# Kernel tuning notes

Measured on AMD Instinct MI355X. Metric: run time of the kernel, lower is better.

The kernel has to match this reference:

```python
import jax, jax.numpy as jnp
import numpy as np

EMBED_DIM = 1024


def setup_inputs() -> dict:
    key = jax.random.key(0)
    ks = jax.random.split(key, 8)
    B, S, D = 4, 2048, EMBED_DIM
    scale = 1.0 / np.sqrt(D)
    x = jax.random.normal(ks[0], (B, S, D), dtype=jnp.float32)
    mask = jnp.zeros((S, S), dtype=jnp.float32)
    # nn.Linear default init ~ U(-1/sqrt(fan_in), 1/sqrt(fan_in)); exact dist irrelevant for correctness
    w_q = jax.random.uniform(ks[1], (D, D), jnp.float32, -scale, scale)
    b_q = jax.random.uniform(ks[2], (D,), jnp.float32, -scale, scale)
    w_k = jax.random.uniform(ks[3], (D, D), jnp.float32, -scale, scale)
    b_k = jax.random.uniform(ks[4], (D,), jnp.float32, -scale, scale)
    w_v = jax.random.uniform(ks[5], (D, D), jnp.float32, -scale, scale)
    b_v = jax.random.uniform(ks[6], (D,), jnp.float32, -scale, scale)
    return {"x": x, "mask": mask, "w_q": w_q, "b_q": b_q,
            "w_k": w_k, "b_k": b_k, "w_v": w_v, "b_v": b_v}


def reference(x, mask, w_q, b_q, w_k, b_k, w_v, b_v):
    D = x.shape[-1]
    # nn.Linear computes x @ W^T + b
    Q = jnp.einsum('bsd,ed->bse', x, w_q) + b_q
    K = jnp.einsum('bsd,ed->bse', x, w_k) + b_k
    V = jnp.einsum('bsd,ed->bse', x, w_v) + b_v
    scores = jnp.einsum('bqd,bkd->bqk', Q, K) / jnp.sqrt(jnp.asarray(D, x.dtype))
    scores = scores + mask  # additive mask, broadcast over batch
    attn = jax.nn.softmax(scores, axis=-1)
    return jnp.einsum('bqk,bkd->bqd', attn, V)
```

## Files before the change

kernel.cpp:

```cpp
#include <hip/hip_runtime.h>


typedef __attribute__((ext_vector_type(8))) short short8;
typedef __attribute__((ext_vector_type(4))) short short4v;
typedef __attribute__((ext_vector_type(4))) float float4v;

__device__ __forceinline__ short f2bf(float f) {
  unsigned u = __builtin_bit_cast(unsigned, f);
  u += 0x7fffu + ((u >> 16) & 1u);
  return (short)(u >> 16);
}
__device__ __forceinline__ float bf2f(short s) {
  unsigned u = ((unsigned)(unsigned short)s) << 16;
  return __builtin_bit_cast(float, u);
}

__device__ __forceinline__ void gl2lds16(const void* g, void* l) {
  __builtin_amdgcn_global_load_lds((const __attribute__((address_space(1))) void*)g,
                                   (__attribute__((address_space(3))) void*)l, 16, 0, 0);
}

__global__ __launch_bounds__(256) void prep_kernel(const float* __restrict__ x,
                                                   const float* __restrict__ wq,
                                                   const float* __restrict__ wk,
                                                   const float* __restrict__ wv,
                                                   const float* __restrict__ bq,
                                                   const float* __restrict__ bk,
                                                   short* __restrict__ x_bf,
                                                   short* __restrict__ w_bf,
                                                   float* __restrict__ bcat) {
  int b = blockIdx.x;
  if (b < 3072) {
    int seg = b >> 10;
    const float* w = seg == 0 ? wq : (seg == 1 ? wk : wv);
    int i = (b - (seg << 10)) * 256 + threadIdx.x;
    float4v v = ((const float4v*)w)[i];
    short4v o;
    o.x = f2bf(v.x); o.y = f2bf(v.y); o.z = f2bf(v.z); o.w = f2bf(v.w);
    ((short4v*)(w_bf + (long)seg * 1048576))[i] = o;
  } else if (b < 11264) {
    int i = (b - 3072) * 256 + threadIdx.x;
    float4v v = ((const float4v*)x)[i];
    short4v o;
    o.x = f2bf(v.x); o.y = f2bf(v.y); o.z = f2bf(v.z); o.w = f2bf(v.w);
    ((short4v*)x_bf)[i] = o;
  } else {
    int i = (b - 11264) * 256 + threadIdx.x;
    if (i < 2048) bcat[i] = i < 1024 ? bq[i] : bk[i - 1024];
  }
}

__device__ __forceinline__ void stage_half(const short* __restrict__ g, int ld,
                                           int grow0, int kt, short* lds, int t) {
  const int r = t >> 3;
  const int cch = (t & 7) ^ (r & 7);
  const long co = (long)kt + cch * 8;
  gl2lds16(g + (long)(grow0 + r) * ld + co, lds + t * 8);
  gl2lds16(g + (long)(grow0 + 64 + r) * ld + co, lds + 4096 + t * 8);
}

template <int EPI>
__device__ __forceinline__ void gemm_body(const short* __restrict__ A,
                                          const short* __restrict__ Bm,
                                          void* __restrict__ C,
                                          const float* __restrict__ aux,
                                          float* __restrict__ rsum, float scale,
                                          int N, int Kd, int Bld, int m0, int n0,
                                          short (*As)[64], short (*Bs)[64]) {
  const int t = threadIdx.x;
  const int lane = t & 63;
  const int wave = t >> 6;
  const int wm = (wave >> 2) * 128;
  const int wn = (wave & 3) * 64;
  const int col = lane & 15, quad = lane >> 4;
  const int sw = col & 7;
  const int NT = Kd >> 6;

  float4v acc[8][4] = {};

  stage_half(A, Kd, m0, 0, &As[0][0], t);
  stage_half(A, Kd, m0 + 128, 0, &As[128][0], t);
  stage_half(Bm, Bld, n0, 0, &Bs[0][0], t);
  stage_half(Bm, Bld, n0 + 128, 0, &Bs[128][0], t);
  if (NT > 1) {
    stage_half(Bm, Bld, n0, 64, &Bs[256][0], t);
    stage_half(Bm, Bld, n0 + 128, 64, &Bs[384][0], t);
    asm volatile("s_waitcnt vmcnt(4)" ::: "memory");
  } else {
    asm volatile("s_waitcnt vmcnt(0)" ::: "memory");
  }
  __builtin_amdgcn_s_barrier();

#pragma unroll 2
  for (int k = 0; k < NT; ++k) {
    const int buf = (k & 1) << 8;
    const int nbf = 256 - buf;
    short8 a[4][2], b0[2][2], b1[2][2];

#pragma unroll
    for (int i = 0; i < 4; ++i)
#pragma unroll
      for (int s = 0; s < 2; ++s)
        a[i][s] = *(const short8*)&As[buf + wm + i * 16 + col][(((s * 4 + quad) ^ sw)) * 8];
#pragma unroll
    for (int j = 0; j < 2; ++j)
#pragma unroll
      for (int s = 0; s < 2; ++s)
        b0[j][s] = *(const short8*)&Bs[buf + wn + j * 16 + col][(((s * 4 + quad) ^ sw)) * 8];
    if (k + 1 < NT) stage_half(A, Kd, m0, (k + 1) * 64, &As[nbf][0], t);
    __builtin_amdgcn_s_barrier();
    __builtin_amdgcn_s_setprio(1);
#pragma unroll
    for (int i = 0; i < 4; ++i)
#pragma unroll
      for (int j = 0; j < 2; ++j)
#pragma unroll
        for (int s = 0; s < 2; ++s)
          acc[i][j] = __builtin_amdgcn_mfma_f32_16x16x32_bf16(a[i][s], b0[j][s], acc[i][j], 0, 0, 0);
    __builtin_amdgcn_s_setprio(0);
    __builtin_amdgcn_s_barrier();

#pragma unroll
    for (int j = 0; j < 2; ++j)
#pragma unroll
      for (int s = 0; s < 2; ++s)
        b1[j][s] = *(const short8*)&Bs[buf + wn + (j + 2) * 16 + col][(((s * 4 + quad) ^ sw)) * 8];
    if (k + 1 < NT) stage_half(A, Kd, m0 + 128, (k + 1) * 64, &As[nbf + 128][0], t);
    __builtin_amdgcn_s_barrier();
    __builtin_amdgcn_s_setprio(1);
#pragma unroll
    for (int i = 0; i < 4; ++i)
#pragma unroll
      for (int j = 0; j < 2; ++j)
#pragma unroll
        for (int s = 0; s < 2; ++s)
          acc[i][j + 2] = __builtin_amdgcn_mfma_f32_16x16x32_bf16(a[i][s], b1[j][s], acc[i][j + 2], 0, 0, 0);
    __builtin_amdgcn_s_setprio(0);
    __builtin_amdgcn_s_barrier();

#pragma unroll
    for (int i = 0; i < 4; ++i)
#pragma unroll
      for (int s = 0; s < 2; ++s)
        a[i][s] = *(const short8*)&As[buf + wm + (i + 4) * 16 + col][(((s * 4 + quad) ^ sw)) * 8];
    if (k + 2 < NT) stage_half(Bm, Bld, n0, (k + 2) * 64, &Bs[buf][0], t);
    __builtin_amdgcn_s_barrier();
    __builtin_amdgcn_s_setprio(1);
#pragma unroll
    for (int i = 0; i < 4; ++i)
#pragma unroll
      for (int j = 0; j < 2; ++j)
#pragma unroll
        for (int s = 0; s < 2; ++s)
          acc[i + 4][j + 2] = __builtin_amdgcn_mfma_f32_16x16x32_bf16(a[i][s], b1[j][s], acc[i + 4][j + 2], 0, 0, 0);
    __builtin_amdgcn_s_setprio(0);
    __builtin_amdgcn_s_barrier();

    if (k + 2 < NT) stage_half(Bm, Bld, n0 + 128, (k + 2) * 64, &Bs[buf + 128][0], t);
    __builtin_amdgcn_s_barrier();
    __builtin_amdgcn_s_setprio(1);
#pragma unroll
    for (int i = 0; i < 4; ++i)
#pragma unroll
      for (int j = 0; j < 2; ++j)
#pragma unroll
        for (int s = 0; s < 2; ++s)
          acc[i + 4][j] = __builtin_amdgcn_mfma_f32_16x16x32_bf16(a[i][s], b0[j][s], acc[i + 4][j], 0, 0, 0);
    __builtin_amdgcn_s_setprio(0);
    if (k + 1 < NT) {
      if (k + 2 < NT) asm volatile("s_waitcnt vmcnt(4)" ::: "memory");
      else            asm volatile("s_waitcnt vmcnt(0)" ::: "memory");
    }
    __builtin_amdgcn_s_barrier();
  }

  float* invb = (float*)&Bs[0][0];
  if (EPI == 2) {
    if (t < 256) {
      float s = 0.f;
#pragma unroll
      for (int p = 0; p < 32; ++p) s += aux[p * 8192 + m0 + t];
      invb[t] = __builtin_amdgcn_rcpf(s);
    }
    __syncthreads();
  }

  const float LOG2E = 1.44269504f;
  const float c1 = scale * LOG2E;
#pragma unroll
  for (int i = 0; i < 8; ++i) {
    float invv[4], addm[4], rsum4[4] = {0.f, 0.f, 0.f, 0.f};
    if (EPI == 2) {
#pragma unroll
      for (int r = 0; r < 4; ++r) invv[r] = invb[wm + i * 16 + quad * 4 + r];
    }
    if (EPI == 3) {
#pragma unroll
      for (int r = 0; r < 4; ++r) addm[r] = aux[m0 + wm + i * 16 + quad * 4 + r];
    }
#pragma unroll
    for (int j = 0; j < 4; ++j) {
      const int n = n0 + wn + j * 16 + col;
      float addn = 0.f;
      if (EPI == 0) addn = aux[n];
#pragma unroll
      for (int r = 0; r < 4; ++r) {
        const int m = m0 + wm + i * 16 + quad * 4 + r;
        float v = acc[i][j][r];
        if (EPI == 0) {
          ((short*)C)[(long)m * N + n] = f2bf(v + addn);
        } else if (EPI == 1) {
          float mv = aux[(long)m * N + n];
          float e = exp2f(fmaf(v, c1, mv * LOG2E));
          short q = f2bf(e);
          ((short*)C)[(long)m * N + n] = q;
          rsum4[r] += bf2f(q);
        } else if (EPI == 2) {
          ((float*)C)[(long)m * N + n] = v * invv[r];
        } else {
          ((short*)C)[(long)m * N + n] = f2bf(v + addm[r]);
        }
      }
    }
    if (EPI == 1) {
#pragma unroll
      for (int r = 0; r < 4; ++r) {
        float s = rsum4[r];
        s += __shfl_xor(s, 1);
        s += __shfl_xor(s, 2);
        s += __shfl_xor(s, 4);
        s += __shfl_xor(s, 8);
        if (col == 0)
          rsum[(wave & 3) * 8192 + m0 + wm + i * 16 + quad * 4 + r] = s;
      }
    }
  }
}

__global__ __launch_bounds__(512, 2) void qkv_kernel(const short* __restrict__ x_bf,
                                                     const short* __restrict__ w_bf,
                                                     short* __restrict__ QK,
                                                     short* __restrict__ Vt,
                                                     const float* __restrict__ bcat,
                                                     const float* __restrict__ bv) {
  __shared__ alignas(16) short As[512][64];
  __shared__ alignas(16) short Bs[512][64];
  const int b = blockIdx.x;
  const int g = (b & 7) * 48 + (b >> 3);
  if (g < 256) {
    const int bz = g >> 7, r = g & 127;
    const int m0 = (r >> 2) * 256, n0 = (r & 3) * 256;
    gemm_body<0>(x_bf, w_bf + (long)bz * 1048576, QK + (long)bz * 8388608,
                 bcat + bz * 1024, nullptr, 1.f, 1024, 1024, 1024, m0, n0, As, Bs);
  } else {
    const int v = g - 256;
    const int m0 = (v >> 5) * 256, n0 = (v & 31) * 256;
    gemm_body<3>(w_bf + 2097152, x_bf, Vt, bv, nullptr, 1.f,
                 8192, 1024, 1024, m0, n0, As, Bs);
  }
}

__global__ __launch_bounds__(512, 2) void scores_kernel(const short* __restrict__ Q,
                                                        const short* __restrict__ Kb,
                                                        short* __restrict__ P,
                                                        const float* __restrict__ mask,
                                                        float* __restrict__ rspart) {
  __shared__ alignas(16) short As[512][64];
  __shared__ alignas(16) short Bs[512][64];
  const int b = blockIdx.x;
  const int g = (b & 7) * 32 + (b >> 3);
  const int bz = g >> 6, t2 = g & 63;
  const int m0 = (t2 >> 3) * 256, n0 = (t2 & 7) * 256;
  gemm_body<1>(Q + (long)bz * 2097152, Kb + (long)bz * 2097152,
               P + (long)bz * 4194304, mask,
               rspart + (long)(n0 >> 8) * 4 * 8192 + bz * 2048, 0.03125f,
               2048, 1024, 1024, m0, n0, As, Bs);
}

__global__ __launch_bounds__(512, 2) void pv_kernel(const short* __restrict__ P,
                                                    const short* __restrict__ Vt,
                                                    float* __restrict__ out,
                                                    const float* __restrict__ rspart) {
  __shared__ alignas(16) short As[512][64];
  __shared__ alignas(16) short Bs[512][64];
  const int b = blockIdx.x;
  const int g = (b & 7) * 16 + (b >> 3);
  const int bz = g >> 5, t2 = g & 31;
  const int m0 = (t2 >> 2) * 256, n0 = (t2 & 3) * 256;
  gemm_body<2>(P + (long)bz * 4194304, Vt + (long)bz * 2048,
               out + (long)bz * 2097152, rspart + bz * 2048, nullptr, 1.f,
               1024, 2048, 8192, m0, n0, As, Bs);
}

extern "C" void kernel_launch(void* const* d_in, const int* in_sizes, int n_in,
                              void* d_out, int out_size, void* d_ws, size_t ws_size,
                              hipStream_t stream) {
  const float* x    = (const float*)d_in[0];
  const float* mask = (const float*)d_in[1];
  const float* wq   = (const float*)d_in[2];
  const float* bq   = (const float*)d_in[3];
  const float* wk   = (const float*)d_in[4];
  const float* bk   = (const float*)d_in[5];
  const float* wv   = (const float*)d_in[6];
  const float* bv   = (const float*)d_in[7];
  float* out = (float*)d_out;

  char* ws = (char*)d_ws;
  const size_t MB = 1024 * 1024;
  short* x_bf   = (short*)(ws);
  float* rspart = (float*)(ws);
  short* w_bf   = (short*)(ws + 16 * MB);
  short* QK     = (short*)(ws + 22 * MB);
  short* Vt     = (short*)(ws + 54 * MB);
  short* P      = (short*)(ws + 70 * MB);
  float* bcat   = (float*)(ws + 70 * MB);

  prep_kernel<<<11272, 256, 0, stream>>>(x, wq, wk, wv, bq, bk, x_bf, w_bf, bcat);

  qkv_kernel<<<384, 512, 0, stream>>>(x_bf, w_bf, QK, Vt, bcat, bv);

  short* Q  = QK;
  short* Kb = QK + 8388608;

  scores_kernel<<<256, 512, 0, stream>>>(Q, Kb, P, mask, rspart);

  pv_kernel<<<128, 512, 0, stream>>>(P, Vt, out, rspart);
}
```

Before: 275.9 us.

## Triple-buffer A tiles in LDS to prefetch two k-steps ahead

```diff
diff --git a/kernel.cpp b/kernel.cpp
--- a/kernel.cpp
+++ b/kernel.cpp
@@ -83,31 +83,34 @@
   stage_half(Bm, Bld, n0, 0, &Bs[0][0], t);
   stage_half(Bm, Bld, n0 + 128, 0, &Bs[128][0], t);
   if (NT > 1) {
+    stage_half(A, Kd, m0, 64, &As[256][0], t);
+    stage_half(A, Kd, m0 + 128, 64, &As[384][0], t);
     stage_half(Bm, Bld, n0, 64, &Bs[256][0], t);
     stage_half(Bm, Bld, n0 + 128, 64, &Bs[384][0], t);
-    asm volatile("s_waitcnt vmcnt(4)" ::: "memory");
+    asm volatile("s_waitcnt vmcnt(8)" ::: "memory");
   } else {
     asm volatile("s_waitcnt vmcnt(0)" ::: "memory");
   }
   __builtin_amdgcn_s_barrier();
 
-#pragma unroll 2
+  int ar = 0;
+  int aw = 512;
+  int br = 0;
+
   for (int k = 0; k < NT; ++k) {
-    const int buf = (k & 1) << 8;
-    const int nbf = 256 - buf;
     short8 a[4][2], b0[2][2], b1[2][2];
 
 #pragma unroll
     for (int i = 0; i < 4; ++i)
 #pragma unroll
       for (int s = 0; s < 2; ++s)
-        a[i][s] = *(const short8*)&As[buf + wm + i * 16 + col][(((s * 4 + quad) ^ sw)) * 8];
+        a[i][s] = *(const short8*)&As[ar + wm + i * 16 + col][(((s * 4 + quad) ^ sw)) * 8];
 #pragma unroll
     for (int j = 0; j < 2; ++j)
 #pragma unroll
       for (int s = 0; s < 2; ++s)
-        b0[j][s] = *(const short8*)&Bs[buf + wn + j * 16 + col][(((s * 4 + quad) ^ sw)) * 8];
-    if (k + 1 < NT) stage_half(A, Kd, m0, (k + 1) * 64, &As[nbf][0], t);
+        b0[j][s] = *(const short8*)&Bs[br + wn + j * 16 + col][(((s * 4 + quad) ^ sw)) * 8];
+    if (k + 2 < NT) stage_half(A, Kd, m0, (k + 2) * 64, &As[aw][0], t);
     __builtin_amdgcn_s_barrier();
     __builtin_amdgcn_s_setprio(1);
 #pragma unroll
@@ -124,8 +127,8 @@
     for (int j = 0; j < 2; ++j)
 #pragma unroll
       for (int s = 0; s < 2; ++s)
-        b1[j][s] = *(const short8*)&Bs[buf + wn + (j + 2) * 16 + col][(((s * 4 + quad) ^ sw)) * 8];
-    if (k + 1 < NT) stage_half(A, Kd, m0 + 128, (k + 1) * 64, &As[nbf + 128][0], t);
+        b1[j][s] = *(const short8*)&Bs[br + wn + (j + 2) * 16 + col][(((s * 4 + quad) ^ sw)) * 8];
+    if (k + 2 < NT) stage_half(A, Kd, m0 + 128, (k + 2) * 64, &As[aw + 128][0], t);
     __builtin_amdgcn_s_barrier();
     __builtin_amdgcn_s_setprio(1);
 #pragma unroll
@@ -142,8 +145,8 @@
     for (int i = 0; i < 4; ++i)
 #pragma unroll
       for (int s = 0; s < 2; ++s)
-        a[i][s] = *(const short8*)&As[buf + wm + (i + 4) * 16 + col][(((s * 4 + quad) ^ sw)) * 8];
-    if (k + 2 < NT) stage_half(Bm, Bld, n0, (k + 2) * 64, &Bs[buf][0], t);
+        a[i][s] = *(const short8*)&As[ar + wm + (i + 4) * 16 + col][(((s * 4 + quad) ^ sw)) * 8];
+    if (k + 2 < NT) stage_half(Bm, Bld, n0, (k + 2) * 64, &Bs[br][0], t);
     __builtin_amdgcn_s_barrier();
     __builtin_amdgcn_s_setprio(1);
 #pragma unroll
@@ -156,7 +159,7 @@
     __builtin_amdgcn_s_setprio(0);
     __builtin_amdgcn_s_barrier();
 
-    if (k + 2 < NT) stage_half(Bm, Bld, n0 + 128, (k + 2) * 64, &Bs[buf + 128][0], t);
+    if (k + 2 < NT) stage_half(Bm, Bld, n0 + 128, (k + 2) * 64, &Bs[br + 128][0], t);
     __builtin_amdgcn_s_barrier();
     __builtin_amdgcn_s_setprio(1);
 #pragma unroll
@@ -167,11 +170,16 @@
         for (int s = 0; s < 2; ++s)
           acc[i + 4][j] = __builtin_amdgcn_mfma_f32_16x16x32_bf16(a[i][s], b0[j][s], acc[i + 4][j], 0, 0, 0);
     __builtin_amdgcn_s_setprio(0);
-    if (k + 1 < NT) {
-      if (k + 2 < NT) asm volatile("s_waitcnt vmcnt(4)" ::: "memory");
-      else            asm volatile("s_waitcnt vmcnt(0)" ::: "memory");
-    }
-    __builtin_amdgcn_s_barrier();
+    if (k + 2 < NT) {
+      asm volatile("s_waitcnt vmcnt(8)" ::: "memory");
+    } else if (k + 1 < NT) {
+      asm volatile("s_waitcnt vmcnt(0)" ::: "memory");
+    }
+    __builtin_amdgcn_s_barrier();
+
+    ar = (ar == 512) ? 0 : ar + 256;
+    aw = (aw == 512) ? 0 : aw + 256;
+    br ^= 256;
   }
 
   float* invb = (float*)&Bs[0][0];
@@ -243,7 +251,7 @@
                                                      short* __restrict__ Vt,
                                                      const float* __restrict__ bcat,
                                                      const float* __restrict__ bv) {
-  __shared__ alignas(16) short As[512][64];
+  __shared__ alignas(16) short As[768][64];
   __shared__ alignas(16) short Bs[512][64];
   const int b = blockIdx.x;
   const int g = (b & 7) * 48 + (b >> 3);
@@ -265,7 +273,7 @@
                                                         short* __restrict__ P,
                                                         const float* __restrict__ mask,
                                                         float* __restrict__ rspart) {
-  __shared__ alignas(16) short As[512][64];
+  __shared__ alignas(16) short As[768][64];
   __shared__ alignas(16) short Bs[512][64];
   const int b = blockIdx.x;
   const int g = (b & 7) * 32 + (b >> 3);
@@ -281,7 +289,7 @@
                                                     const short* __restrict__ Vt,
                                                     float* __restrict__ out,
                                                     const float* __restrict__ rspart) {
-  __shared__ alignas(16) short As[512][64];
+  __shared__ alignas(16) short As[768][64];
   __shared__ alignas(16) short Bs[512][64];
   const int b = blockIdx.x;
   const int g = (b & 7) * 16 + (b >> 3);
```

After: 273.1 us. Within noise of the previous version (-1.0%).
